# Kernel tuning notes

Hardware: AMD Instinct MI355X
Metric: run time of the kernel (lower is better)

Reference implementation:

```python
import jax, jax.numpy as jnp
import numpy as np

N_NODES = 100000
N_EDGES = 1600000


def setup_inputs() -> dict:
    key = jax.random.key(0)
    k1, k2, k3, k4 = jax.random.split(key, 4)
    x = jax.random.normal(k1, (N_NODES, 128), dtype=jnp.float32)
    edge_index = jax.random.randint(k2, (2, N_EDGES), 0, N_NODES, dtype=jnp.int64)
    # Glorot-ish init for weights
    W1 = jax.random.normal(k3, (128, 128), dtype=jnp.float32) * (1.0 / np.sqrt(128))
    b1 = jnp.zeros((128,), dtype=jnp.float32)
    W2 = jax.random.normal(k4, (128, 64), dtype=jnp.float32) * (1.0 / np.sqrt(128))
    b2 = jnp.zeros((64,), dtype=jnp.float32)
    return {"x": x, "edge_index": edge_index, "W1": W1, "b1": b1, "W2": W2, "b2": b2}


def _gcn_conv(x, src, dst, W, b):
    """PyG GCNConv: h = W x; symmetric deg^-1/2 norm over edges (incl. self-loops); scatter-add; + bias."""
    n = x.shape[0]
    h = x @ W  # [N, out]
    ones = jnp.ones(src.shape[0], dtype=h.dtype)
    deg = jax.ops.segment_sum(ones, dst, num_segments=n)  # in-degree incl self-loops
    dinv = jax.lax.rsqrt(jnp.maximum(deg, 1e-12))
    norm = dinv[src] * dinv[dst]  # [E+N]
    msg = h[src] * norm[:, None]  # [E+N, out] gather
    out = jax.ops.segment_sum(msg, dst, num_segments=n)  # scatter-add
    return out + b


def reference(x, edge_index, W1, b1, W2, b2):
    n = x.shape[0]
    loop = jnp.arange(n, dtype=edge_index.dtype)
    src = jnp.concatenate([edge_index[0], loop])  # add self-loops
    dst = jnp.concatenate([edge_index[1], loop])
    h = jax.nn.relu(_gcn_conv(x, src, dst, W1, b1))
    # dropout is identity in eval mode
    return _gcn_conv(h, src, dst, W2, b2)
```

## Files before the change

kernel.cpp:

```cpp
#include <hip/hip_runtime.h>
#include <hip/hip_bf16.h>

#define THREADS 256
#define BSHIFT 9
#define BIN_CHUNK 4096
#define KP 136

typedef __attribute__((ext_vector_type(8))) short bf16x8;
typedef __attribute__((ext_vector_type(4))) float f32x4;


__device__ inline unsigned short f2bf(float f) {
    unsigned int u = __float_as_uint(f);
    unsigned int r = (u + 0x7fffu + ((u >> 16) & 1u)) >> 16;
    return (unsigned short)r;
}

__device__ inline float2 bf2_to_f2(unsigned int u) {
    float2 r;
    r.x = __uint_as_float(u << 16);
    r.y = __uint_as_float(u & 0xffff0000u);
    return r;
}

__device__ inline void accum_row(float* acc, uint4 v) {
    float2 a = bf2_to_f2(v.x), b = bf2_to_f2(v.y), c = bf2_to_f2(v.z), d = bf2_to_f2(v.w);
    acc[0] += a.x; acc[1] += a.y; acc[2] += b.x; acc[3] += b.y;
    acc[4] += c.x; acc[5] += c.y; acc[6] += d.x; acc[7] += d.y;
}

__device__ inline void accum_row_scaled(float* acc, uint4 v, float s) {
    float2 a = bf2_to_f2(v.x), b = bf2_to_f2(v.y), c = bf2_to_f2(v.z), d = bf2_to_f2(v.w);
    acc[0] = fmaf(s, a.x, acc[0]); acc[1] = fmaf(s, a.y, acc[1]);
    acc[2] = fmaf(s, b.x, acc[2]); acc[3] = fmaf(s, b.y, acc[3]);
    acc[4] = fmaf(s, c.x, acc[4]); acc[5] = fmaf(s, c.y, acc[5]);
    acc[6] = fmaf(s, d.x, acc[6]); acc[7] = fmaf(s, d.y, acc[7]);
}


__global__ __launch_bounds__(256) void k_bin_gemm1(const int* __restrict__ src,
                                                   const int* __restrict__ dst,
                                                   int* __restrict__ bcur,
                                                   unsigned int* __restrict__ binned,
                                                   int E, int NB, int cap,
                                                   const float* __restrict__ x,
                                                   const float* __restrict__ W1,
                                                   unsigned short* __restrict__ h,
                                                   int M, int nbin) {
    __shared__ __align__(16) char smem[64 * KP * 2 + 128 * KP * 2];
    const int t = threadIdx.x;

    if ((int)blockIdx.x < nbin) {
        int* bcnt = (int*)smem;
        int* bres = bcnt + 256;
        bcnt[t] = 0;
        __syncthreads();
        int base = blockIdx.x * BIN_CHUNK;
        int sv[16], dv[16];
#pragma unroll
        for (int i = 0; i < 16; ++i) {
            int e = base + t + i * 256;
            if (e < E) {
                sv[i] = src[e];
                dv[i] = dst[e];
                atomicAdd(&bcnt[dv[i] >> BSHIFT], 1);
            } else {
                dv[i] = -1;
            }
        }
        __syncthreads();
        if (t < NB) {
            int old = bcnt[t] ? atomicAdd(&bcur[t], bcnt[t]) : 0;
            bres[t] = t * cap + old;
        }
        __syncthreads();
#pragma unroll
        for (int i = 0; i < 16; ++i) {
            if (dv[i] >= 0) {
                int b = dv[i] >> BSHIFT;
                int pos = atomicAdd(&bres[b], 1);
                if (pos < (b + 1) * cap)
                    binned[pos] = ((unsigned int)(dv[i] & 511) << 23) | (unsigned int)sv[i];
            }
        }
        return;
    }

    short* As = (short*)smem;
    short* Bs = (short*)(smem + 64 * KP * 2);
    const int m0 = ((int)blockIdx.x - nbin) * 64;

    {
        int ar = t >> 5;
        int ac = (t & 31) * 4;
#pragma unroll
        for (int rb = 0; rb < 64; rb += 8) {
            int lrow = rb + ar;
            int row = m0 + lrow;
            ushort4 sv = make_ushort4(0, 0, 0, 0);
            if (row < M) {
                float4 v = *(const float4*)(x + (size_t)row * 128 + ac);
                sv.x = f2bf(v.x); sv.y = f2bf(v.y); sv.z = f2bf(v.z); sv.w = f2bf(v.w);
            }
            *(ushort4*)&As[lrow * KP + ac] = sv;
        }
    }
    {
        int bk = t / 32;
        int bn = (t % 32) * 4;
#pragma unroll
        for (int kb = 0; kb < 128; kb += 8) {
            int k = kb + bk;
            float4 wv = *(const float4*)(W1 + (size_t)k * 128 + bn);
            Bs[(bn + 0) * KP + k] = f2bf(wv.x);
            Bs[(bn + 1) * KP + k] = f2bf(wv.y);
            Bs[(bn + 2) * KP + k] = f2bf(wv.z);
            Bs[(bn + 3) * KP + k] = f2bf(wv.w);
        }
    }
    __syncthreads();

    const int w = t >> 6;
    const int lane = t & 63;
    const int lm = lane & 15;
    const int qd = lane >> 4;
    const int n0w = w * 32;

    f32x4 acc[4][2];
#pragma unroll
    for (int mi = 0; mi < 4; ++mi)
#pragma unroll
        for (int ni = 0; ni < 2; ++ni) acc[mi][ni] = (f32x4){0.f, 0.f, 0.f, 0.f};

#pragma unroll
    for (int ks = 0; ks < 4; ++ks) {
        bf16x8 a[4], b[2];
#pragma unroll
        for (int mi = 0; mi < 4; ++mi)
            a[mi] = *(const bf16x8*)&As[(mi * 16 + lm) * KP + ks * 32 + qd * 8];
#pragma unroll
        for (int ni = 0; ni < 2; ++ni)
            b[ni] = *(const bf16x8*)&Bs[(n0w + ni * 16 + lm) * KP + ks * 32 + qd * 8];
#pragma unroll
        for (int mi = 0; mi < 4; ++mi)
#pragma unroll
            for (int ni = 0; ni < 2; ++ni)
                acc[mi][ni] = __builtin_amdgcn_mfma_f32_16x16x32_bf16(a[mi], b[ni], acc[mi][ni], 0, 0, 0);
    }

#pragma unroll
    for (int mi = 0; mi < 4; ++mi) {
#pragma unroll
        for (int ni = 0; ni < 2; ++ni) {
            int col = n0w + ni * 16 + lm;
#pragma unroll
            for (int r = 0; r < 4; ++r) {
                int lrow = mi * 16 + qd * 4 + r;
                int row = m0 + lrow;
                if (row < M) h[(size_t)row * 128 + col] = f2bf(acc[mi][ni][r]);
            }
        }
    }
}

__global__ __launch_bounds__(256) void k_node_place(const unsigned int* __restrict__ binned,
                                                    const int* __restrict__ bcur, int cap,
                                                    int* __restrict__ rp,
                                                    int* __restrict__ deg,
                                                    float* __restrict__ dinv,
                                                    int* __restrict__ eperm, int N) {
    __shared__ int lc[512];
    __shared__ int s[256];
    int b = blockIdx.x;
    int t = threadIdx.x;
    int beg = b * cap;
    int end = beg + min(bcur[b], cap);
    int d0 = b << BSHIFT;
    lc[t] = 0;
    lc[t + 256] = 0;
    __syncthreads();
    for (int j = beg + t; j < end; j += 256) atomicAdd(&lc[binned[j] >> 23], 1);
    __syncthreads();
    int a = lc[2 * t], c = lc[2 * t + 1];
    int pair = a + c;
    s[t] = pair;
    __syncthreads();
    for (int off = 1; off < 256; off <<= 1) {
        int add = (t >= off) ? s[t - off] : 0;
        __syncthreads();
        s[t] += add;
        __syncthreads();
    }
    int excl = s[t] - pair;
    int st0 = beg + excl, st1 = st0 + a;
    int node0 = d0 + 2 * t;
    if (node0 < N) {
        rp[node0] = st0;
        deg[node0] = a;
        dinv[node0] = rsqrtf((float)a + 1.0f);
    }
    if (node0 + 1 < N) {
        rp[node0 + 1] = st1;
        deg[node0 + 1] = c;
        dinv[node0 + 1] = rsqrtf((float)c + 1.0f);
    }
    __syncthreads();
    lc[2 * t] = st0;
    lc[2 * t + 1] = st1;
    __syncthreads();
    for (int j = beg + t; j < end; j += 256) {
        unsigned int p = binned[j];
        int pos = atomicAdd(&lc[p >> 23], 1);
        eperm[pos] = (int)(p & 0x7fffffu);
    }
}


__global__ __launch_bounds__(256) void k_gather_gemm2(const int* __restrict__ rp,
                                                      const int* __restrict__ deg,
                                                      const int* __restrict__ eperm,
                                                      const float* __restrict__ dinv,
                                                      const uint4* __restrict__ h4,
                                                      const float* __restrict__ b1,
                                                      const float* __restrict__ W2,
                                                      unsigned short* __restrict__ h2,
                                                      int n) {
    __shared__ short As[64 * KP];
    __shared__ short Bs[64 * KP];
    __shared__ float sDin[64];

    const int t = threadIdx.x;
    const int lane = t & 63;
    const int l16 = lane & 15;
    const int gbase = lane & 48;
    const int m0 = blockIdx.x * 64;

    {
        int bk = t / 16;
        int bn = (t % 16) * 4;
#pragma unroll
        for (int kb = 0; kb < 128; kb += 16) {
            int k = kb + bk;
            float4 wv = *(const float4*)(W2 + (size_t)k * 64 + bn);
            Bs[(bn + 0) * KP + k] = f2bf(wv.x);
            Bs[(bn + 1) * KP + k] = f2bf(wv.y);
            Bs[(bn + 2) * KP + k] = f2bf(wv.z);
            Bs[(bn + 3) * KP + k] = f2bf(wv.w);
        }
    }
    if (t < 64) sDin[t] = (m0 + t < n) ? dinv[m0 + t] : 1.0f;

#pragma unroll 1
    for (int r = 0; r < 4; ++r) {
        const int lrow = r * 16 + ((t >> 6) << 2) + (lane >> 4);
        const int node = m0 + lrow;
        const bool valid = node < n;

        int beg = 0, end = 0;
        float dv_self = 0.f;
        if (valid) {
            beg = rp[node];
            end = beg + deg[node];
            dv_self = dinv[node];
        }

        float acc[8];
#pragma unroll
        for (int i = 0; i < 8; ++i) acc[i] = 0.f;
        if (valid) accum_row_scaled(acc, h4[(size_t)node * 16 + l16], dv_self);

        for (int j = beg; j < end; j += 16) {
            int cnt = end - j;
            if (cnt > 16) cnt = 16;
            int ep = eperm[j + (l16 < cnt ? l16 : cnt - 1)];
            float dvv = dinv[ep];
            int k = 0;
            for (; k + 4 <= cnt; k += 4) {
                int i0 = __shfl(ep, gbase + k);
                int i1 = __shfl(ep, gbase + k + 1);
                int i2 = __shfl(ep, gbase + k + 2);
                int i3 = __shfl(ep, gbase + k + 3);
                float d0 = __shfl(dvv, gbase + k);
                float d1 = __shfl(dvv, gbase + k + 1);
                float d2 = __shfl(dvv, gbase + k + 2);
                float d3 = __shfl(dvv, gbase + k + 3);
                uint4 v0 = h4[(size_t)i0 * 16 + l16];
                uint4 v1 = h4[(size_t)i1 * 16 + l16];
                uint4 v2 = h4[(size_t)i2 * 16 + l16];
                uint4 v3 = h4[(size_t)i3 * 16 + l16];
                accum_row_scaled(acc, v0, d0);
                accum_row_scaled(acc, v1, d1);
                accum_row_scaled(acc, v2, d2);
                accum_row_scaled(acc, v3, d3);
            }
            for (; k < cnt; ++k) {
                int i0 = __shfl(ep, gbase + k);
                float d0 = __shfl(dvv, gbase + k);
                uint4 v0 = h4[(size_t)i0 * 16 + l16];
                accum_row_scaled(acc, v0, d0);
            }
        }

        float4 bb0 = ((const float4*)b1)[l16 * 2];
        float4 bb1 = ((const float4*)b1)[l16 * 2 + 1];
        float o0 = fmaxf(fmaf(dv_self, acc[0], bb0.x), 0.f);
        float o1 = fmaxf(fmaf(dv_self, acc[1], bb0.y), 0.f);
        float o2 = fmaxf(fmaf(dv_self, acc[2], bb0.z), 0.f);
        float o3 = fmaxf(fmaf(dv_self, acc[3], bb0.w), 0.f);
        float o4 = fmaxf(fmaf(dv_self, acc[4], bb1.x), 0.f);
        float o5 = fmaxf(fmaf(dv_self, acc[5], bb1.y), 0.f);
        float o6 = fmaxf(fmaf(dv_self, acc[6], bb1.z), 0.f);
        float o7 = fmaxf(fmaf(dv_self, acc[7], bb1.w), 0.f);
        ushort4 s0 = make_ushort4(f2bf(o0), f2bf(o1), f2bf(o2), f2bf(o3));
        ushort4 s1 = make_ushort4(f2bf(o4), f2bf(o5), f2bf(o6), f2bf(o7));
        *(ushort4*)&As[lrow * KP + l16 * 8] = s0;
        *(ushort4*)&As[lrow * KP + l16 * 8 + 4] = s1;
    }
    __syncthreads();

    const int w = t >> 6;
    const int lm = lane & 15;
    const int qd = lane >> 4;
    const int n0w = w * 16;

    f32x4 c4[4];
#pragma unroll
    for (int mi = 0; mi < 4; ++mi) c4[mi] = (f32x4){0.f, 0.f, 0.f, 0.f};

#pragma unroll
    for (int ks = 0; ks < 4; ++ks) {
        bf16x8 a[4], b;
#pragma unroll
        for (int mi = 0; mi < 4; ++mi)
            a[mi] = *(const bf16x8*)&As[(mi * 16 + lm) * KP + ks * 32 + qd * 8];
        b = *(const bf16x8*)&Bs[(n0w + lm) * KP + ks * 32 + qd * 8];
#pragma unroll
        for (int mi = 0; mi < 4; ++mi)
            c4[mi] = __builtin_amdgcn_mfma_f32_16x16x32_bf16(a[mi], b, c4[mi], 0, 0, 0);
    }

#pragma unroll
    for (int mi = 0; mi < 4; ++mi) {
        int col = n0w + lm;
#pragma unroll
        for (int r = 0; r < 4; ++r) {
            int lrow = mi * 16 + qd * 4 + r;
            int row = m0 + lrow;
            if (row < n) h2[(size_t)row * 64 + col] = f2bf(sDin[lrow] * c4[mi][r]);
        }
    }
}

__global__ __launch_bounds__(256) void k_gather64(const int* __restrict__ rp,
                                                  const int* __restrict__ deg,
                                                  const int* __restrict__ eperm,
                                                  const float* __restrict__ dinv,
                                                  const uint4* __restrict__ h4,
                                                  const float* __restrict__ bias,
                                                  float* __restrict__ out, int n) {
    const int t = threadIdx.x;
    const int lane = t & 63;
    const int l8 = lane & 7;
    const int gbase = lane & 56;
    const int node = blockIdx.x * 32 + (t >> 6) * 8 + (lane >> 3);
    const bool valid = node < n;

    int beg = 0, end = 0;
    if (valid) {
        beg = rp[node];
        end = beg + deg[node];
    }

    float acc[8];
#pragma unroll
    for (int i = 0; i < 8; ++i) acc[i] = 0.f;
    if (valid) accum_row(acc, h4[(size_t)node * 8 + l8]);

    int j = beg;
    for (; j + 16 <= end; j += 16) {
        int ep0 = eperm[j + l8];
        int ep1 = eperm[j + 8 + l8];
        int idx[16];
#pragma unroll
        for (int k = 0; k < 8; ++k) idx[k] = __shfl(ep0, gbase + k);
#pragma unroll
        for (int k = 0; k < 8; ++k) idx[8 + k] = __shfl(ep1, gbase + k);
        uint4 v[16];
#pragma unroll
        for (int k = 0; k < 16; ++k) v[k] = h4[(size_t)idx[k] * 8 + l8];
#pragma unroll
        for (int k = 0; k < 16; ++k) accum_row(acc, v[k]);
    }
    int cnt = end - j;
    if (cnt >= 8) {
        int ep = eperm[j + l8];
        int idx[8];
#pragma unroll
        for (int k = 0; k < 8; ++k) idx[k] = __shfl(ep, gbase + k);
        uint4 v[8];
#pragma unroll
        for (int k = 0; k < 8; ++k) v[k] = h4[(size_t)idx[k] * 8 + l8];
#pragma unroll
        for (int k = 0; k < 8; ++k) accum_row(acc, v[k]);
        j += 8;
        cnt -= 8;
    }
    if (cnt > 0) {
        int ep = eperm[j + (l8 < cnt ? l8 : cnt - 1)];
        int k = 0;
        for (; k + 4 <= cnt; k += 4) {
            int i0 = __shfl(ep, gbase + k);
            int i1 = __shfl(ep, gbase + k + 1);
            int i2 = __shfl(ep, gbase + k + 2);
            int i3 = __shfl(ep, gbase + k + 3);
            uint4 v0 = h4[(size_t)i0 * 8 + l8];
            uint4 v1 = h4[(size_t)i1 * 8 + l8];
            uint4 v2 = h4[(size_t)i2 * 8 + l8];
            uint4 v3 = h4[(size_t)i3 * 8 + l8];
            accum_row(acc, v0);
            accum_row(acc, v1);
            accum_row(acc, v2);
            accum_row(acc, v3);
        }
        for (; k < cnt; ++k) {
            int i0 = __shfl(ep, gbase + k);
            uint4 v0 = h4[(size_t)i0 * 8 + l8];
            accum_row(acc, v0);
        }
    }

    if (valid) {
        float dv = dinv[node];
        float4 b0 = ((const float4*)bias)[l8 * 2];
        float4 b1 = ((const float4*)bias)[l8 * 2 + 1];
        float4 o0, o1;
        o0.x = dv * acc[0] + b0.x; o0.y = dv * acc[1] + b0.y;
        o0.z = dv * acc[2] + b0.z; o0.w = dv * acc[3] + b0.w;
        o1.x = dv * acc[4] + b1.x; o1.y = dv * acc[5] + b1.y;
        o1.z = dv * acc[6] + b1.z; o1.w = dv * acc[7] + b1.w;
        float4* orow = (float4*)(out + (size_t)node * 64);
        orow[l8 * 2] = o0;
        orow[l8 * 2 + 1] = o1;
    }
}


extern "C" void kernel_launch(void* const* d_in, const int* in_sizes, int n_in,
                              void* d_out, int out_size, void* d_ws, size_t ws_size,
                              hipStream_t stream) {
    const float* x  = (const float*)d_in[0];
    const int*   ei = (const int*)d_in[1];
    const float* W1 = (const float*)d_in[2];
    const float* b1 = (const float*)d_in[3];
    const float* W2 = (const float*)d_in[4];
    const float* b2 = (const float*)d_in[5];
    float* out = (float*)d_out;

    const int N = in_sizes[0] / 128;
    const int E = in_sizes[1] / 2;
    const int* src = ei;
    const int* dst = ei + E;
    const int NB = (N + 511) >> BSHIFT;
    const int cap = (E + NB - 1) / NB + ((E / NB) >> 2) + 1024;

    char* ws = (char*)d_ws;
    size_t off = 0;
    auto carve = [&](size_t bytes) -> void* {
        void* p = ws + off;
        off = (off + bytes + 255) & ~(size_t)255;
        return p;
    };
    float* dinv = (float*)carve((size_t)N * 4);
    int*   rp   = (int*)carve((size_t)N * 4);
    int*   deg  = (int*)carve((size_t)N * 4);
    int*   bcur = (int*)carve(256 * 4);
    unsigned int* binned = (unsigned int*)carve((size_t)NB * cap * 4);
    int*   eperm = (int*)carve((size_t)NB * cap * 4);
    unsigned short* h  = (unsigned short*)carve((size_t)N * 128 * 2);
    unsigned short* h2 = (unsigned short*)carve((size_t)N * 128 * 2);

    const int gMm = (N + 63) / 64;
    const int nbin = (E + BIN_CHUNK - 1) / BIN_CHUNK;

    hipMemsetAsync(bcur, 0, 256 * sizeof(int), stream);
    k_bin_gemm1<<<nbin + gMm, THREADS, 0, stream>>>(src, dst, bcur, binned, E, NB, cap,
                                                    x, W1, h, N, nbin);
    k_node_place<<<NB, THREADS, 0, stream>>>(binned, bcur, cap, rp, deg, dinv, eperm, N);

    k_gather_gemm2<<<gMm, THREADS, 0, stream>>>(rp, deg, eperm, dinv, (const uint4*)h, b1, W2, h2, N);

    k_gather64<<<(N + 31) / 32, THREADS, 0, stream>>>(rp, deg, eperm, dinv, (const uint4*)h2, b2, out, N);
}
```

Baseline: 275.0 us.

## Load weight fragments directly from global memory instead of staging in LDS

Both GEMM kernels stop staging the bf16-converted weight matrix in shared memory. Each wave now loads its MFMA B fragments straight from global (cached) memory with scalar strided loads and converts them in registers. This roughly halves LDS use per block and removes a transposing LDS write pass, which should allow more blocks per CU, and k_gather_gemm2 now requests 8 blocks per CU through launch bounds. The cost is redundant, uncoalesced global loads of the weights in every block, plus a per-row dinv global load in the epilogue where the values used to come from shared memory.

```diff
diff --git a/kernel.cpp b/kernel.cpp
--- a/kernel.cpp
+++ b/kernel.cpp
@@ -7,6 +7,7 @@
 #define KP 136
 
 typedef __attribute__((ext_vector_type(8))) short bf16x8;
+typedef __attribute__((ext_vector_type(8))) unsigned short u16x8;
 typedef __attribute__((ext_vector_type(4))) float f32x4;
 
 
@@ -35,6 +36,13 @@
     acc[2] = fmaf(s, b.x, acc[2]); acc[3] = fmaf(s, b.y, acc[3]);
     acc[4] = fmaf(s, c.x, acc[4]); acc[5] = fmaf(s, c.y, acc[5]);
     acc[6] = fmaf(s, d.x, acc[6]); acc[7] = fmaf(s, d.y, acc[7]);
+}
+
+__device__ inline bf16x8 load_bfrag(const float* __restrict__ W, int ldn, int k0, int col) {
+    bf16x8 b;
+#pragma unroll
+    for (int i = 0; i < 8; ++i) b[i] = (short)f2bf(W[(size_t)(k0 + i) * ldn + col]);
+    return b;
 }
 
 
@@ -47,11 +55,11 @@
                                                    const float* __restrict__ W1,
                                                    unsigned short* __restrict__ h,
                                                    int M, int nbin) {
-    __shared__ __align__(16) char smem[64 * KP * 2 + 128 * KP * 2];
+    __shared__ __align__(16) short As[64 * KP];
     const int t = threadIdx.x;
 
     if ((int)blockIdx.x < nbin) {
-        int* bcnt = (int*)smem;
+        int* bcnt = (int*)As;
         int* bres = bcnt + 256;
         bcnt[t] = 0;
         __syncthreads();
@@ -86,10 +94,7 @@
         return;
     }
 
-    short* As = (short*)smem;
-    short* Bs = (short*)(smem + 64 * KP * 2);
     const int m0 = ((int)blockIdx.x - nbin) * 64;
-
     {
         int ar = t >> 5;
         int ac = (t & 31) * 4;
@@ -105,19 +110,6 @@
             *(ushort4*)&As[lrow * KP + ac] = sv;
         }
     }
-    {
-        int bk = t / 32;
-        int bn = (t % 32) * 4;
-#pragma unroll
-        for (int kb = 0; kb < 128; kb += 8) {
-            int k = kb + bk;
-            float4 wv = *(const float4*)(W1 + (size_t)k * 128 + bn);
-            Bs[(bn + 0) * KP + k] = f2bf(wv.x);
-            Bs[(bn + 1) * KP + k] = f2bf(wv.y);
-            Bs[(bn + 2) * KP + k] = f2bf(wv.z);
-            Bs[(bn + 3) * KP + k] = f2bf(wv.w);
-        }
-    }
     __syncthreads();
 
     const int w = t >> 6;
@@ -134,18 +126,14 @@
 
 #pragma unroll
     for (int ks = 0; ks < 4; ++ks) {
-        bf16x8 a[4], b[2];
-#pragma unroll
-        for (int mi = 0; mi < 4; ++mi)
-            a[mi] = *(const bf16x8*)&As[(mi * 16 + lm) * KP + ks * 32 + qd * 8];
-#pragma unroll
-        for (int ni = 0; ni < 2; ++ni)
-            b[ni] = *(const bf16x8*)&Bs[(n0w + ni * 16 + lm) * KP + ks * 32 + qd * 8];
-#pragma unroll
-        for (int mi = 0; mi < 4; ++mi)
-#pragma unroll
-            for (int ni = 0; ni < 2; ++ni)
-                acc[mi][ni] = __builtin_amdgcn_mfma_f32_16x16x32_bf16(a[mi], b[ni], acc[mi][ni], 0, 0, 0);
+        bf16x8 b0 = load_bfrag(W1, 128, ks * 32 + qd * 8, n0w + lm);
+        bf16x8 b1 = load_bfrag(W1, 128, ks * 32 + qd * 8, n0w + 16 + lm);
+#pragma unroll
+        for (int mi = 0; mi < 4; ++mi) {
+            bf16x8 a = *(const bf16x8*)&As[(mi * 16 + lm) * KP + ks * 32 + qd * 8];
+            acc[mi][0] = __builtin_amdgcn_mfma_f32_16x16x32_bf16(a, b0, acc[mi][0], 0, 0, 0);
+            acc[mi][1] = __builtin_amdgcn_mfma_f32_16x16x32_bf16(a, b1, acc[mi][1], 0, 0, 0);
+        }
     }
 
 #pragma unroll
@@ -216,39 +204,22 @@
 }
 
 
-__global__ __launch_bounds__(256) void k_gather_gemm2(const int* __restrict__ rp,
-                                                      const int* __restrict__ deg,
-                                                      const int* __restrict__ eperm,
-                                                      const float* __restrict__ dinv,
-                                                      const uint4* __restrict__ h4,
-                                                      const float* __restrict__ b1,
-                                                      const float* __restrict__ W2,
-                                                      unsigned short* __restrict__ h2,
-                                                      int n) {
-    __shared__ short As[64 * KP];
-    __shared__ short Bs[64 * KP];
-    __shared__ float sDin[64];
+__global__ __launch_bounds__(256, 8) void k_gather_gemm2(const int* __restrict__ rp,
+                                                         const int* __restrict__ deg,
+                                                         const int* __restrict__ eperm,
+                                                         const float* __restrict__ dinv,
+                                                         const uint4* __restrict__ h4,
+                                                         const float* __restrict__ b1,
+                                                         const float* __restrict__ W2,
+                                                         unsigned short* __restrict__ h2,
+                                                         int n) {
+    __shared__ __align__(16) short As[64 * KP];
 
     const int t = threadIdx.x;
     const int lane = t & 63;
     const int l16 = lane & 15;
     const int gbase = lane & 48;
     const int m0 = blockIdx.x * 64;
-
-    {
-        int bk = t / 16;
-        int bn = (t % 16) * 4;
-#pragma unroll
-        for (int kb = 0; kb < 128; kb += 16) {
-            int k = kb + bk;
-            float4 wv = *(const float4*)(W2 + (size_t)k * 64 + bn);
-            Bs[(bn + 0) * KP + k] = f2bf(wv.x);
-            Bs[(bn + 1) * KP + k] = f2bf(wv.y);
-            Bs[(bn + 2) * KP + k] = f2bf(wv.z);
-            Bs[(bn + 3) * KP + k] = f2bf(wv.w);
-        }
-    }
-    if (t < 64) sDin[t] = (m0 + t < n) ? dinv[m0 + t] : 1.0f;
 
 #pragma unroll 1
     for (int r = 0; r < 4; ++r) {
@@ -303,25 +274,25 @@
 
         float4 bb0 = ((const float4*)b1)[l16 * 2];
         float4 bb1 = ((const float4*)b1)[l16 * 2 + 1];
-        float o0 = fmaxf(fmaf(dv_self, acc[0], bb0.x), 0.f);
-        float o1 = fmaxf(fmaf(dv_self, acc[1], bb0.y), 0.f);
-        float o2 = fmaxf(fmaf(dv_self, acc[2], bb0.z), 0.f);
-        float o3 = fmaxf(fmaf(dv_self, acc[3], bb0.w), 0.f);
-        float o4 = fmaxf(fmaf(dv_self, acc[4], bb1.x), 0.f);
-        float o5 = fmaxf(fmaf(dv_self, acc[5], bb1.y), 0.f);
-        float o6 = fmaxf(fmaf(dv_self, acc[6], bb1.z), 0.f);
-        float o7 = fmaxf(fmaf(dv_self, acc[7], bb1.w), 0.f);
-        ushort4 s0 = make_ushort4(f2bf(o0), f2bf(o1), f2bf(o2), f2bf(o3));
-        ushort4 s1 = make_ushort4(f2bf(o4), f2bf(o5), f2bf(o6), f2bf(o7));
-        *(ushort4*)&As[lrow * KP + l16 * 8] = s0;
-        *(ushort4*)&As[lrow * KP + l16 * 8 + 4] = s1;
-    }
-    __syncthreads();
+        u16x8 s;
+        s[0] = f2bf(fmaxf(fmaf(dv_self, acc[0], bb0.x), 0.f));
+        s[1] = f2bf(fmaxf(fmaf(dv_self, acc[1], bb0.y), 0.f));
+        s[2] = f2bf(fmaxf(fmaf(dv_self, acc[2], bb0.z), 0.f));
+        s[3] = f2bf(fmaxf(fmaf(dv_self, acc[3], bb0.w), 0.f));
+        s[4] = f2bf(fmaxf(fmaf(dv_self, acc[4], bb1.x), 0.f));
+        s[5] = f2bf(fmaxf(fmaf(dv_self, acc[5], bb1.y), 0.f));
+        s[6] = f2bf(fmaxf(fmaf(dv_self, acc[6], bb1.z), 0.f));
+        s[7] = f2bf(fmaxf(fmaf(dv_self, acc[7], bb1.w), 0.f));
+        *(u16x8*)&As[lrow * KP + l16 * 8] = s;
+    }
+    __syncthreads();
+    __builtin_amdgcn_sched_barrier(0);
 
     const int w = t >> 6;
     const int lm = lane & 15;
     const int qd = lane >> 4;
     const int n0w = w * 16;
+    const int col = n0w + lm;
 
     f32x4 c4[4];
 #pragma unroll
@@ -329,24 +300,21 @@
 
 #pragma unroll
     for (int ks = 0; ks < 4; ++ks) {
-        bf16x8 a[4], b;
-#pragma unroll
-        for (int mi = 0; mi < 4; ++mi)
-            a[mi] = *(const bf16x8*)&As[(mi * 16 + lm) * KP + ks * 32 + qd * 8];
-        b = *(const bf16x8*)&Bs[(n0w + lm) * KP + ks * 32 + qd * 8];
-#pragma unroll
-        for (int mi = 0; mi < 4; ++mi)
-            c4[mi] = __builtin_amdgcn_mfma_f32_16x16x32_bf16(a[mi], b, c4[mi], 0, 0, 0);
+        bf16x8 b = load_bfrag(W2, 64, ks * 32 + qd * 8, col);
+#pragma unroll
+        for (int mi = 0; mi < 4; ++mi) {
+            bf16x8 a = *(const bf16x8*)&As[(mi * 16 + lm) * KP + ks * 32 + qd * 8];
+            c4[mi] = __builtin_amdgcn_mfma_f32_16x16x32_bf16(a, b, c4[mi], 0, 0, 0);
+        }
     }
 
 #pragma unroll
     for (int mi = 0; mi < 4; ++mi) {
-        int col = n0w + lm;
 #pragma unroll
         for (int r = 0; r < 4; ++r) {
             int lrow = mi * 16 + qd * 4 + r;
             int row = m0 + lrow;
-            if (row < n) h2[(size_t)row * 64 + col] = f2bf(sDin[lrow] * c4[mi][r]);
+            if (row < n) h2[(size_t)row * 64 + col] = f2bf(dinv[row] * c4[mi][r]);
         }
     }
 }
```

Result: faster. 266.7 us (-3.0%).
